# Performance work log

Hardware: AMD Instinct MI355X
Metric: run time of the kernel (lower is better)

The kernel has to match this reference:

```python
import jax, jax.numpy as jnp
import numpy as np

EMBED_DIM = 1024


def setup_inputs() -> dict:
    key = jax.random.key(0)
    ks = jax.random.split(key, 9)
    d = EMBED_DIM
    s = 1.0 / np.sqrt(d)
    x = jax.random.normal(ks[0], (4, 4096, d), dtype=jnp.float32)
    Wq = jax.random.normal(ks[1], (d, d), dtype=jnp.float32) * s
    bq = jax.random.normal(ks[2], (d,), dtype=jnp.float32) * 0.01
    Wk = jax.random.normal(ks[3], (d, d), dtype=jnp.float32) * s
    bk = jax.random.normal(ks[4], (d,), dtype=jnp.float32) * 0.01
    Wv = jax.random.normal(ks[5], (d, d), dtype=jnp.float32) * s
    bv = jax.random.normal(ks[6], (d,), dtype=jnp.float32) * 0.01
    Wo = jax.random.normal(ks[7], (d, d), dtype=jnp.float32) * s
    bo = jax.random.normal(ks[8], (d,), dtype=jnp.float32) * 0.01
    return {"x": x, "Wq": Wq, "bq": bq, "Wk": Wk, "bk": bk,
            "Wv": Wv, "bv": bv, "Wo": Wo, "bo": bo}


def reference(x, Wq, bq, Wk, bk, Wv, bv, Wo, bo):
    # x: [b, s, d]; single-head attention, scale = 1/sqrt(d)
    b, s, d = x.shape
    q = x @ Wq + bq
    k = x @ Wk + bk
    v = x @ Wv + bv
    scale = 1.0 / jnp.sqrt(jnp.asarray(d, x.dtype))
    scores = jnp.einsum('bqd,bkd->bqk', q, k) * scale  # [b, s, s]
    causal = jnp.tril(jnp.ones((s, s), dtype=bool))
    scores = jnp.where(causal, scores, jnp.asarray(-jnp.inf, scores.dtype))
    attn = jax.nn.softmax(scores, axis=-1)
    ctx = jnp.einsum('bqk,bkd->bqd', attn, v)
    return ctx @ Wo + bo
```

## Files before the change

kernel.cpp:

```cpp
#include <hip/hip_runtime.h>


typedef unsigned short u16;
typedef __attribute__((ext_vector_type(4))) unsigned short u16x4;
typedef __attribute__((ext_vector_type(8))) unsigned short u16x8;
typedef __attribute__((ext_vector_type(8))) __bf16 bf16x8;
typedef __attribute__((ext_vector_type(4))) float f32x4;

typedef const __attribute__((address_space(1))) void* as1cp;
typedef __attribute__((address_space(3))) void* as3p;

#define SBAR() __builtin_amdgcn_s_barrier()
#define SPIN() __builtin_amdgcn_sched_barrier(0)

struct GemmPtrs {
  const u16* A[4];
  const u16* B[4];
  const float* bias[4];
  void* C[4];
};
struct TransPtrs {
  const void* in[4];
  u16* out[4];
};
struct SmPtrs {
  u16* P[4];
};

__device__ __forceinline__ u16 f2bf(float f) {
  union { float f; unsigned int i; } c; c.f = f;
  unsigned int r = c.i + 0x7fffu + ((c.i >> 16) & 1u);
  return (u16)(r >> 16);
}
__device__ __forceinline__ float bf2f(u16 u) {
  union { unsigned int i; float f; } c; c.i = ((unsigned int)u) << 16;
  return c.f;
}

__global__ __launch_bounds__(256) void cast_f32_bf16(const float* __restrict__ in,
                                                     u16* __restrict__ out, int n4) {
  int i = blockIdx.x * blockDim.x + threadIdx.x;
  if (i >= n4) return;
  float4 v = ((const float4*)in)[i];
  u16x4 u;
  u.x = f2bf(v.x); u.y = f2bf(v.y); u.z = f2bf(v.z); u.w = f2bf(v.w);
  ((u16x4*)out)[i] = u;
}

template <bool IN_F32>
__global__ __launch_bounds__(256) void transpose_to_bf16(TransPtrs tp, int R, int C) {
  __shared__ u16 t[32][34];
  int z = blockIdx.z;
  int tx = threadIdx.x, ty = threadIdx.y;
  int c0 = blockIdx.x * 32, r0 = blockIdx.y * 32;
#pragma unroll
  for (int dy = 0; dy < 4; ++dy) {
    int r = r0 + ty + dy * 8;
    int c = c0 + tx;
    u16 hv;
    if (IN_F32) hv = f2bf(((const float*)tp.in[z])[(size_t)r * C + c]);
    else        hv = ((const u16*)tp.in[z])[(size_t)r * C + c];
    t[ty + dy * 8][tx] = hv;
  }
  __syncthreads();
  u16* op = tp.out[z];
#pragma unroll
  for (int dy = 0; dy < 4; ++dy) {
    int a = ty + dy * 8;
    op[(size_t)(c0 + a) * R + r0 + tx] = t[tx][a];
  }
}

__global__ __launch_bounds__(256) void softmax_causal(SmPtrs sp) {
  int row = blockIdx.x;
  u16* P = sp.P[blockIdx.y];
  int tid = threadIdx.x;
  int lane = tid & 63, wv = tid >> 6;
  u16x8* prow = (u16x8*)(P + (size_t)row * 4096);
  int nch = (row >> 3) + 1;
  int fend = ((row >> 7) + 1) << 4;
  int c0 = tid, c1 = tid + 256;
  bool a0 = c0 < nch, a1 = c1 < nch;
  float vals[16];
  float lmax = -3.0e38f;
  if (a0) {
    u16x8 u = prow[c0];
#pragma unroll
    for (int e = 0; e < 8; ++e) {
      float f = (c0 * 8 + e <= row) ? bf2f(u[e]) : -3.0e38f;
      vals[e] = f; lmax = fmaxf(lmax, f);
    }
  } else {
#pragma unroll
    for (int e = 0; e < 8; ++e) vals[e] = -3.0e38f;
  }
  if (a1) {
    u16x8 u = prow[c1];
#pragma unroll
    for (int e = 0; e < 8; ++e) {
      float f = (c1 * 8 + e <= row) ? bf2f(u[e]) : -3.0e38f;
      vals[8 + e] = f; lmax = fmaxf(lmax, f);
    }
  } else {
#pragma unroll
    for (int e = 0; e < 8; ++e) vals[8 + e] = -3.0e38f;
  }
  __shared__ float red[8];
#pragma unroll
  for (int off = 32; off > 0; off >>= 1) lmax = fmaxf(lmax, __shfl_down(lmax, off, 64));
  if (lane == 0) red[wv] = lmax;
  __syncthreads();
  float m2 = fmaxf(fmaxf(red[0], red[1]), fmaxf(red[2], red[3]));
  float lsum = 0.f;
#pragma unroll
  for (int e = 0; e < 16; ++e) {
    float ev = __expf(vals[e] - m2);
    vals[e] = ev;
    lsum += ev;
  }
#pragma unroll
  for (int off = 32; off > 0; off >>= 1) lsum += __shfl_down(lsum, off, 64);
  if (lane == 0) red[4 + wv] = lsum;
  __syncthreads();
  float inv = 1.0f / (red[4] + red[5] + red[6] + red[7]);
  if (a0) {
    u16x8 u;
#pragma unroll
    for (int e = 0; e < 8; ++e) u[e] = f2bf(vals[e] * inv);
    prow[c0] = u;
  }
  if (a1) {
    u16x8 u;
#pragma unroll
    for (int e = 0; e < 8; ++e) u[e] = f2bf(vals[8 + e] * inv);
    prow[c1] = u;
  }
  u16x8 zz = (u16x8)(u16)0;
  for (int c = nch + tid; c < fend; c += 256) prow[c] = zz;
}

template <int MODE, bool OUT_BF16, bool HAS_BIAS>
__global__ __launch_bounds__(512, 2) void gemm8ph(GemmPtrs p, int N, float cscale) {
  __shared__ __align__(16) u16 As[3][8192];
  __shared__ __align__(16) u16 Bs[3][8192];
  const int b = blockIdx.x;
  const int tid = threadIdx.x, lane = tid & 63, wv = tid >> 6;
  const int wm = (wv >> 2) << 7, wn = (wv & 3) << 6;
  const int lrow = lane & 15, lquad = lane >> 4;
  const int xs = (lquad ^ ((lrow >> 1) & 3)) << 3;
  const int aoff0 = (wm + lrow) * 32 + xs;
  const int boff0 = (wn + lrow) * 32 + xs;
  const int soff = (tid >> 2) * 1024 + (((tid & 3) ^ ((tid >> 3) & 3)) << 3);
  const int x = b & 7, u = b >> 3;
  const int nslot = (MODE == 1) ? (u < 4 ? 3 : 2) : (MODE == 0 ? 3 : 1);

  struct TP { const u16* A; const u16* B; int tm, tn, z; };
  auto tileOf = [&](int s) {
    TP t;
    if (MODE == 0) {
      int i = x * 32 + u;
      t.z = s; t.tm = (i >> 2) << 8; t.tn = (i & 3) << 8;
    } else if (MODE == 1) {
      int g = x * 68 + s * 32 + u;
      t.z = g / 136; int L = g - t.z * 136;
      int i = (int)((__fsqrt_rn(8.f * (float)L + 1.f) - 1.f) * 0.5f);
      while ((i + 1) * (i + 2) / 2 <= L) ++i;
      while (i * (i + 1) / 2 > L) --i;
      t.tm = i << 8; t.tn = (L - ((i * (i + 1)) >> 1)) << 8;
    } else {
      int i = x * 32 + u;
      t.z = 0; t.tm = (i >> 2) << 8; t.tn = (i & 3) << 8;
    }
    t.A = p.A[t.z] + (size_t)t.tm * 1024;
    t.B = p.B[t.z] + (size_t)t.tn * 1024;
    return t;
  };

  const u16* gA; const u16* gB; int stk = 0, sslot = 0;
  {
    TP t0 = tileOf(0);
    gA = t0.A + soff; gB = t0.B + soff;
  }
  auto adv = [&]() {
    gA += 32; gB += 32;
    if (++stk == 32) {
      stk = 0;
      if (++sslot < nslot) {
        TP t = tileOf(sslot);
        gA = t.A + soff; gB = t.B + soff;
      }
    }
  };
  auto stgA = [&](int s) __attribute__((always_inline)) {
    __builtin_amdgcn_global_load_lds((as1cp)gA, (as3p)(As[s] + wv * 512), 16, 0, 0);
    __builtin_amdgcn_global_load_lds((as1cp)(gA + 131072), (as3p)(As[s] + 4096 + wv * 512), 16, 0, 0);
  };
  auto stgB = [&](int s) __attribute__((always_inline)) {
    __builtin_amdgcn_global_load_lds((as1cp)gB, (as3p)(Bs[s] + wv * 512), 16, 0, 0);
    __builtin_amdgcn_global_load_lds((as1cp)(gB + 131072), (as3p)(Bs[s] + 4096 + wv * 512), 16, 0, 0);
    adv();
  };

  f32x4 acc[8][4];
#pragma unroll
  for (int i = 0; i < 8; ++i)
#pragma unroll
    for (int j = 0; j < 4; ++j) acc[i][j] = (f32x4){0.f, 0.f, 0.f, 0.f};

  auto epi = [&](int cs2) {
    TP t = tileOf(cs2);
    float bvv[4] = {0.f, 0.f, 0.f, 0.f};
    if constexpr (HAS_BIAS) {
#pragma unroll
      for (int n = 0; n < 4; ++n) bvv[n] = p.bias[t.z][t.tn + wn + n * 16 + lrow];
    }
#pragma unroll
    for (int m = 0; m < 8; ++m)
#pragma unroll
      for (int r = 0; r < 4; ++r) {
        size_t row = (size_t)(t.tm + wm + m * 16 + lquad * 4 + r);
#pragma unroll
        for (int n = 0; n < 4; ++n) {
          int col = t.tn + wn + n * 16 + lrow;
          float vvv = acc[m][n][r] * cscale + bvv[n];
          if (OUT_BF16) ((u16*)p.C[t.z])[row * N + col] = f2bf(vvv);
          else          ((float*)p.C[t.z])[row * N + col] = vvv;
        }
      }
#pragma unroll
    for (int m2 = 0; m2 < 8; ++m2)
#pragma unroll
      for (int n2 = 0; n2 < 4; ++n2) acc[m2][n2] = (f32x4){0.f, 0.f, 0.f, 0.f};
  };

  stgA(0); stgB(0);
  stgA(1); stgB(1);
  asm volatile("s_waitcnt vmcnt(4)");
  SBAR();
  SPIN();

  const int T = nslot * 32;
  int cs = 0, c = 0;
  for (int t = 0; t < T; ++t) {
    const int s = (c >= 1) ? c - 1 : 2;
    const bool stg = (t + 2) < T;
    bf16x8 af[4], bf[4];
#pragma unroll
    for (int m = 0; m < 4; ++m) af[m] = *(const bf16x8*)&As[c][aoff0 + m * 512];
#pragma unroll
    for (int n = 0; n < 4; ++n) bf[n] = *(const bf16x8*)&Bs[c][boff0 + n * 512];
    if (stg) stgA(s);
    SPIN();
    SBAR();
    asm volatile("s_waitcnt lgkmcnt(0)");
    SPIN();
    __builtin_amdgcn_s_setprio(1);
#pragma unroll
    for (int m = 0; m < 4; ++m)
#pragma unroll
      for (int n = 0; n < 4; ++n)
        acc[m][n] = __builtin_amdgcn_mfma_f32_16x16x32_bf16(af[m], bf[n], acc[m][n], 0, 0, 0);
    __builtin_amdgcn_s_setprio(0);
    SPIN();
    SBAR();
#pragma unroll
    for (int m = 0; m < 4; ++m) af[m] = *(const bf16x8*)&As[c][aoff0 + 2048 + m * 512];
    if (stg) stgB(s);
    SPIN();
    if (stg)               asm volatile("s_waitcnt vmcnt(4)");
    else if (t + 1 < T)    asm volatile("s_waitcnt vmcnt(0)");
    SBAR();
    asm volatile("s_waitcnt lgkmcnt(0)");
    SPIN();
    __builtin_amdgcn_s_setprio(1);
#pragma unroll
    for (int m = 0; m < 4; ++m)
#pragma unroll
      for (int n = 0; n < 4; ++n)
        acc[4 + m][n] = __builtin_amdgcn_mfma_f32_16x16x32_bf16(af[m], bf[n], acc[4 + m][n], 0, 0, 0);
    __builtin_amdgcn_s_setprio(0);
    SPIN();
    SBAR();
    if (((t + 1) & 31) == 0) { SPIN(); epi(cs); ++cs; }
    if (++c == 3) c = 0;
  }
}

__global__ __launch_bounds__(512, 2) void gemm_pv3(GemmPtrs p) {
  __shared__ __align__(16) u16 As[3][4096];
  __shared__ __align__(16) u16 Bs[3][8192];
  const int b = blockIdx.x;
  const int tid = threadIdx.x, lane = tid & 63, wv = tid >> 6;
  const int wm = (wv >> 2) << 6, wn = (wv & 3) << 6;
  const int lrow = lane & 15, lquad = lane >> 4;
  const int xs = (lquad ^ ((lrow >> 1) & 3)) << 3;
  const int aoff0 = (wm + lrow) * 32 + xs;
  const int boff0 = (wn + lrow) * 32 + xs;
  const int soff = (tid >> 2) * 4096 + (((tid & 3) ^ ((tid >> 3) & 3)) << 3);
  const int x = b & 7, u = b >> 3;
  const int P = x * 32 + u;
  const int z = P >> 6, j = (P >> 2) & 15, n4 = P & 3;
  const int i1 = j, i2 = 31 - j;
  const int tn = n4 << 8;
  const int T1 = (i1 + 1) * 4;
  const int niter1 = (i2 + 1) * 4;
  const u16* Abase = p.A[z];
  const u16* Bbase = p.B[z] + (size_t)tn * 4096;

  const u16* gA = Abase + (size_t)(i1 << 7) * 4096 + soff;
  const u16* gB = Bbase + soff;
  int stk = 0, sslot = 0;
  auto adv = [&]() {
    gA += 32; gB += 32;
    ++stk;
    if (sslot == 0 && stk == T1) {
      stk = 0; sslot = 1;
      gA = Abase + (size_t)(i2 << 7) * 4096 + soff;
      gB = Bbase + soff;
    } else if (sslot == 1 && stk == niter1) {
      stk = 0; sslot = 2;
    }
  };
  auto stage = [&](int s) __attribute__((always_inline)) {
    __builtin_amdgcn_global_load_lds((as1cp)gA, (as3p)(As[s] + wv * 512), 16, 0, 0);
    __builtin_amdgcn_global_load_lds((as1cp)gB, (as3p)(Bs[s] + wv * 512), 16, 0, 0);
    __builtin_amdgcn_global_load_lds((as1cp)(gB + 524288), (as3p)(Bs[s] + 4096 + wv * 512), 16, 0, 0);
    adv();
  };

  f32x4 acc[4][4];
#pragma unroll
  for (int i = 0; i < 4; ++i)
#pragma unroll
    for (int jj = 0; jj < 4; ++jj) acc[i][jj] = (f32x4){0.f, 0.f, 0.f, 0.f};

  auto epi = [&](int s) {
    int tm = (s ? i2 : i1) << 7;
#pragma unroll
    for (int m = 0; m < 4; ++m)
#pragma unroll
      for (int r = 0; r < 4; ++r) {
        size_t row = (size_t)(tm + wm + m * 16 + lquad * 4 + r);
#pragma unroll
        for (int n = 0; n < 4; ++n) {
          int col = tn + wn + n * 16 + lrow;
          ((u16*)p.C[z])[row * 1024 + col] = f2bf(acc[m][n][r]);
        }
      }
#pragma unroll
    for (int m2 = 0; m2 < 4; ++m2)
#pragma unroll
      for (int n2 = 0; n2 < 4; ++n2) acc[m2][n2] = (f32x4){0.f, 0.f, 0.f, 0.f};
  };

  stage(0); stage(1);
  asm volatile("s_waitcnt vmcnt(3)");
  SBAR();
  SPIN();

  const int T = 132;
  int c = 0;
  for (int t = 0; t < T; ++t) {
    const int s = (c >= 1) ? c - 1 : 2;
    const bool stg = (t + 2) < T;
    bf16x8 af[4], bf[4];
#pragma unroll
    for (int m = 0; m < 4; ++m) af[m] = *(const bf16x8*)&As[c][aoff0 + m * 512];
#pragma unroll
    for (int n = 0; n < 4; ++n) bf[n] = *(const bf16x8*)&Bs[c][boff0 + n * 512];
    if (stg) stage(s);
    SPIN();
    if (stg)            asm volatile("s_waitcnt vmcnt(3)");
    else if (t + 1 < T) asm volatile("s_waitcnt vmcnt(0)");
    SBAR();
    asm volatile("s_waitcnt lgkmcnt(0)");
    SPIN();
    __builtin_amdgcn_s_setprio(1);
#pragma unroll
    for (int m = 0; m < 4; ++m)
#pragma unroll
      for (int n = 0; n < 4; ++n)
        acc[m][n] = __builtin_amdgcn_mfma_f32_16x16x32_bf16(af[m], bf[n], acc[m][n], 0, 0, 0);
    __builtin_amdgcn_s_setprio(0);
    SPIN();
    SBAR();
    if (t + 1 == T1) { SPIN(); epi(0); }
    if (++c == 3) c = 0;
  }
  epi(1);
}

extern "C" void kernel_launch(void* const* d_in, const int* in_sizes, int n_in,
                              void* d_out, int out_size, void* d_ws, size_t ws_size,
                              hipStream_t stream) {
  const float* x  = (const float*)d_in[0];
  const float* Wq = (const float*)d_in[1];
  const float* bq = (const float*)d_in[2];
  const float* Wk = (const float*)d_in[3];
  const float* bk = (const float*)d_in[4];
  const float* Wv = (const float*)d_in[5];
  const float* bv = (const float*)d_in[6];
  const float* Wo = (const float*)d_in[7];
  const float* bo = (const float*)d_in[8];

  const int S = 4096, D = 1024;
  const size_t XE = (size_t)4 * S * D;
  const size_t BSE = (size_t)S * D;

  char* ws = (char*)d_ws;
  u16* xb  = (u16*)(ws + 0);
  u16* q   = (u16*)(ws + 33554432);
  u16* k   = (u16*)(ws + 67108864);
  u16* v   = (u16*)(ws + 100663296);
  u16* ctx = (u16*)(ws + 134217728);
  u16* wqT = (u16*)(ws + 167772160);
  u16* wkT = wqT + 1048576;
  u16* wvT = wkT + 1048576;
  u16* woT = wvT + 1048576;
  u16* attn2 = (u16*)(ws + 176160768);
  u16* attn0 = (u16*)d_out;
  u16* attn1 = attn0 + (size_t)S * S;
  u16* attn3 = v;
  u16* vT = xb;
  u16* attn[4] = {attn0, attn1, attn2, attn3};

  cast_f32_bf16<<<(int)(XE / 4 / 256), 256, 0, stream>>>(x, xb, (int)(XE / 4));
  {
    TransPtrs tp = {{Wq, Wk, Wv, Wo}, {wqT, wkT, wvT, woT}};
    transpose_to_bf16<true><<<dim3(32, 32, 4), dim3(32, 8), 0, stream>>>(tp, D, D);
  }
  {
    GemmPtrs gp = {{xb, xb, xb, xb}, {wqT, wkT, wvT, wqT},
                   {bq, bk, bv, bq}, {q, k, v, q}};
    gemm8ph<0, true, true><<<256, 512, 0, stream>>>(gp, D, 1.0f);
  }
  {
    TransPtrs tp = {{v, v + BSE, v + 2 * BSE, v + 3 * BSE},
                    {vT, vT + BSE, vT + 2 * BSE, vT + 3 * BSE}};
    transpose_to_bf16<false><<<dim3(D / 32, S / 32, 4), dim3(32, 8), 0, stream>>>(tp, S, D);
  }
  {
    GemmPtrs gp = {{q, q + BSE, q + 2 * BSE, q + 3 * BSE},
                   {k, k + BSE, k + 2 * BSE, k + 3 * BSE},
                   {nullptr, nullptr, nullptr, nullptr},
                   {attn[0], attn[1], attn[2], attn[3]}};
    gemm8ph<1, true, false><<<256, 512, 0, stream>>>(gp, S, 0.03125f);
  }
  {
    SmPtrs sp = {{attn[0], attn[1], attn[2], attn[3]}};
    softmax_causal<<<dim3(S, 4), 256, 0, stream>>>(sp);
  }
  {
    GemmPtrs gp = {{attn[0], attn[1], attn[2], attn[3]},
                   {vT, vT + BSE, vT + 2 * BSE, vT + 3 * BSE},
                   {nullptr, nullptr, nullptr, nullptr},
                   {ctx, ctx + BSE, ctx + 2 * BSE, ctx + 3 * BSE}};
    gemm_pv3<<<256, 512, 0, stream>>>(gp);
  }
  {
    GemmPtrs gp = {{ctx, ctx, ctx, ctx}, {woT, woT, woT, woT},
                   {bo, bo, bo, bo}, {d_out, d_out, d_out, d_out}};
    gemm8ph<3, false, true><<<256, 512, 0, stream>>>(gp, D, 1.0f);
  }
}
```

Baseline: 508.3 us.

## Fuse causal softmax into QK epilogue and PV prologue with per-tile statistics

Removes the standalone softmax pass over the score matrix. The QK GEMM epilogue now computes per-row, per-256-column-block max and sum-of-exp. A small combine kernel merges these into a row max and inverse sum. The PV GEMM then loads raw scores through registers, applies exp, normalisation and the causal mask, and writes the result to LDS before the MFMAs. This avoids a full read-modify-write of the bf16 score matrix. The cost is extra work in the epilogue (reductions, barriers) and exp work in the PV main loop, whose A operand is no longer staged with direct global-to-LDS async loads.

```diff
diff --git a/kernel.cpp b/kernel.cpp
--- a/kernel.cpp
+++ b/kernel.cpp
@@ -23,9 +23,6 @@
   const void* in[4];
   u16* out[4];
 };
-struct SmPtrs {
-  u16* P[4];
-};
 
 __device__ __forceinline__ u16 f2bf(float f) {
   union { float f; unsigned int i; } c; c.f = f;
@@ -71,78 +68,32 @@
   }
 }
 
-__global__ __launch_bounds__(256) void softmax_causal(SmPtrs sp) {
-  int row = blockIdx.x;
-  u16* P = sp.P[blockIdx.y];
-  int tid = threadIdx.x;
-  int lane = tid & 63, wv = tid >> 6;
-  u16x8* prow = (u16x8*)(P + (size_t)row * 4096);
-  int nch = (row >> 3) + 1;
-  int fend = ((row >> 7) + 1) << 4;
-  int c0 = tid, c1 = tid + 256;
-  bool a0 = c0 < nch, a1 = c1 < nch;
-  float vals[16];
-  float lmax = -3.0e38f;
-  if (a0) {
-    u16x8 u = prow[c0];
-#pragma unroll
-    for (int e = 0; e < 8; ++e) {
-      float f = (c0 * 8 + e <= row) ? bf2f(u[e]) : -3.0e38f;
-      vals[e] = f; lmax = fmaxf(lmax, f);
-    }
-  } else {
-#pragma unroll
-    for (int e = 0; e < 8; ++e) vals[e] = -3.0e38f;
-  }
-  if (a1) {
-    u16x8 u = prow[c1];
-#pragma unroll
-    for (int e = 0; e < 8; ++e) {
-      float f = (c1 * 8 + e <= row) ? bf2f(u[e]) : -3.0e38f;
-      vals[8 + e] = f; lmax = fmaxf(lmax, f);
-    }
-  } else {
-#pragma unroll
-    for (int e = 0; e < 8; ++e) vals[8 + e] = -3.0e38f;
-  }
-  __shared__ float red[8];
-#pragma unroll
-  for (int off = 32; off > 0; off >>= 1) lmax = fmaxf(lmax, __shfl_down(lmax, off, 64));
-  if (lane == 0) red[wv] = lmax;
-  __syncthreads();
-  float m2 = fmaxf(fmaxf(red[0], red[1]), fmaxf(red[2], red[3]));
-  float lsum = 0.f;
-#pragma unroll
-  for (int e = 0; e < 16; ++e) {
-    float ev = __expf(vals[e] - m2);
-    vals[e] = ev;
-    lsum += ev;
-  }
-#pragma unroll
-  for (int off = 32; off > 0; off >>= 1) lsum += __shfl_down(lsum, off, 64);
-  if (lane == 0) red[4 + wv] = lsum;
-  __syncthreads();
-  float inv = 1.0f / (red[4] + red[5] + red[6] + red[7]);
-  if (a0) {
-    u16x8 u;
-#pragma unroll
-    for (int e = 0; e < 8; ++e) u[e] = f2bf(vals[e] * inv);
-    prow[c0] = u;
-  }
-  if (a1) {
-    u16x8 u;
-#pragma unroll
-    for (int e = 0; e < 8; ++e) u[e] = f2bf(vals[8 + e] * inv);
-    prow[c1] = u;
-  }
-  u16x8 zz = (u16x8)(u16)0;
-  for (int c = nch + tid; c < fend; c += 256) prow[c] = zz;
+__global__ __launch_bounds__(256) void sm_combine(const float* __restrict__ gM,
+                                                  const float* __restrict__ gS,
+                                                  float* __restrict__ Mrow,
+                                                  float* __restrict__ Linv) {
+  int r = blockIdx.x * 256 + threadIdx.x;
+  int z = r >> 12, row = r & 4095;
+  int nb = (row >> 8) + 1;
+  float M = -3.0e38f;
+  for (int cb = 0; cb < nb; ++cb)
+    M = fmaxf(M, gM[(((z * 16 + cb) << 12)) + row]);
+  float L = 0.f;
+  for (int cb = 0; cb < nb; ++cb) {
+    float pm = gM[(((z * 16 + cb) << 12)) + row];
+    L += gS[(((z * 16 + cb) << 12)) + row] * __expf(pm - M);
+  }
+  Mrow[(z << 12) + row] = M;
+  Linv[(z << 12) + row] = 1.0f / L;
 }
 
 template <int MODE, bool OUT_BF16, bool HAS_BIAS>
-__global__ __launch_bounds__(512, 2) void gemm8ph(GemmPtrs p, int N, float cscale) {
+__global__ __launch_bounds__(512, 2) void gemm8ph(GemmPtrs p, int N, float cscale,
+                                                  float* gM, float* gS) {
   __shared__ __align__(16) u16 As[3][8192];
   __shared__ __align__(16) u16 Bs[3][8192];
+  __shared__ __align__(16) float smax[1024];
+  __shared__ __align__(16) float ssum[1024];
   const int b = blockIdx.x;
   const int tid = threadIdx.x, lane = tid & 63, wv = tid >> 6;
   const int wm = (wv >> 2) << 7, wn = (wv & 3) << 6;
@@ -209,6 +160,65 @@
 
   auto epi = [&](int cs2) {
     TP t = tileOf(cs2);
+    if constexpr (MODE == 1) {
+      const bool diag = (t.tm == t.tn);
+      const int wnidx = wv & 3;
+#pragma unroll
+      for (int m = 0; m < 8; ++m)
+#pragma unroll
+        for (int r = 0; r < 4; ++r) {
+          int rl = wm + m * 16 + lquad * 4 + r;
+          float mx = -3.0e38f;
+#pragma unroll
+          for (int n = 0; n < 4; ++n) {
+            float vb = bf2f(f2bf(acc[m][n][r] * cscale));
+            int cl = wn + n * 16 + lrow;
+            if (diag && cl > rl) vb = -3.0e38f;
+            mx = fmaxf(mx, vb);
+          }
+          mx = fmaxf(mx, __shfl_xor(mx, 1, 64));
+          mx = fmaxf(mx, __shfl_xor(mx, 2, 64));
+          mx = fmaxf(mx, __shfl_xor(mx, 4, 64));
+          mx = fmaxf(mx, __shfl_xor(mx, 8, 64));
+          if (lrow == 0) smax[rl * 4 + wnidx] = mx;
+        }
+      SBAR();
+#pragma unroll
+      for (int m = 0; m < 8; ++m)
+#pragma unroll
+        for (int r = 0; r < 4; ++r) {
+          int rl = wm + m * 16 + lquad * 4 + r;
+          f32x4 m4 = *(const f32x4*)&smax[rl * 4];
+          float Mt = fmaxf(fmaxf(m4[0], m4[1]), fmaxf(m4[2], m4[3]));
+          float sm = 0.f;
+#pragma unroll
+          for (int n = 0; n < 4; ++n) {
+            float vb = bf2f(f2bf(acc[m][n][r] * cscale));
+            int cl = wn + n * 16 + lrow;
+            if (diag && cl > rl) vb = -3.0e38f;
+            sm += __expf(vb - Mt);
+          }
+          sm += __shfl_xor(sm, 1, 64); sm += __shfl_xor(sm, 2, 64);
+          sm += __shfl_xor(sm, 4, 64); sm += __shfl_xor(sm, 8, 64);
+          if (lrow == 0) ssum[rl * 4 + wnidx] = sm;
+        }
+      SBAR();
+      if ((wv & 3) == 0) {
+#pragma unroll
+        for (int h = 0; h < 2; ++h) {
+          int rl = wm + h * 64 + lane;
+          f32x4 m4 = *(const f32x4*)&smax[rl * 4];
+          float Mt = fmaxf(fmaxf(m4[0], m4[1]), fmaxf(m4[2], m4[3]));
+          f32x4 s4 = *(const f32x4*)&ssum[rl * 4];
+          float L = (s4[0] + s4[1]) + (s4[2] + s4[3]);
+          int row_abs = t.tm + rl;
+          int cb = t.tn >> 8;
+          gM[((t.z * 16 + cb) << 12) + row_abs] = Mt;
+          gS[((t.z * 16 + cb) << 12) + row_abs] = L;
+        }
+      }
+      SBAR();
+    }
     float bvv[4] = {0.f, 0.f, 0.f, 0.f};
     if constexpr (HAS_BIAS) {
 #pragma unroll
@@ -286,7 +296,9 @@
   }
 }
 
-__global__ __launch_bounds__(512, 2) void gemm_pv3(GemmPtrs p) {
+__global__ __launch_bounds__(512, 2) void gemm_pvf(GemmPtrs p,
+                                                   const float* __restrict__ Mrow,
+                                                   const float* __restrict__ Linv) {
   __shared__ __align__(16) u16 As[3][4096];
   __shared__ __align__(16) u16 Bs[3][8192];
   const int b = blockIdx.x;
@@ -296,36 +308,57 @@
   const int xs = (lquad ^ ((lrow >> 1) & 3)) << 3;
   const int aoff0 = (wm + lrow) * 32 + xs;
   const int boff0 = (wn + lrow) * 32 + xs;
-  const int soff = (tid >> 2) * 4096 + (((tid & 3) ^ ((tid >> 3) & 3)) << 3);
+  const int jsw = (((tid & 3) ^ ((tid >> 3) & 3)) << 3);
+  const int soffB = (tid >> 2) * 4096 + jsw;
   const int x = b & 7, u = b >> 3;
   const int P = x * 32 + u;
   const int z = P >> 6, j = (P >> 2) & 15, n4 = P & 3;
   const int i1 = j, i2 = 31 - j;
   const int tn = n4 << 8;
   const int T1 = (i1 + 1) * 4;
-  const int niter1 = (i2 + 1) * 4;
+  const int T = 132;
+  const int T2 = T - T1;
   const u16* Abase = p.A[z];
   const u16* Bbase = p.B[z] + (size_t)tn * 4096;
 
-  const u16* gA = Abase + (size_t)(i1 << 7) * 4096 + soff;
-  const u16* gB = Bbase + soff;
-  int stk = 0, sslot = 0;
+  const int rloc = tid >> 2;
+  const int ra1 = (i1 << 7) + rloc, ra2 = (i2 << 7) + rloc;
+  const float M1 = Mrow[(z << 12) + ra1], L1i = Linv[(z << 12) + ra1];
+  const float M2 = Mrow[(z << 12) + ra2], L2i = Linv[(z << 12) + ra2];
+
+  const u16* gA = Abase + (size_t)ra1 * 4096 + jsw;
+  const u16* gB = Bbase + soffB;
+  int stk = 0;
   auto adv = [&]() {
     gA += 32; gB += 32;
-    ++stk;
-    if (sslot == 0 && stk == T1) {
-      stk = 0; sslot = 1;
-      gA = Abase + (size_t)(i2 << 7) * 4096 + soff;
-      gB = Bbase + soff;
-    } else if (sslot == 1 && stk == niter1) {
-      stk = 0; sslot = 2;
-    }
-  };
-  auto stage = [&](int s) __attribute__((always_inline)) {
-    __builtin_amdgcn_global_load_lds((as1cp)gA, (as3p)(As[s] + wv * 512), 16, 0, 0);
+    if (++stk == T1) {
+      gA = Abase + (size_t)ra2 * 4096 + jsw;
+      gB = Bbase + soffB;
+    }
+  };
+  auto stgB = [&](int s) __attribute__((always_inline)) {
     __builtin_amdgcn_global_load_lds((as1cp)gB, (as3p)(Bs[s] + wv * 512), 16, 0, 0);
     __builtin_amdgcn_global_load_lds((as1cp)(gB + 524288), (as3p)(Bs[s] + 4096 + wv * 512), 16, 0, 0);
-    adv();
+  };
+
+  auto xform = [&](int kt, int slot, u16x8 a8) __attribute__((always_inline)) {
+    const bool s2 = (kt >= T1);
+    const int klocal = s2 ? kt - T1 : kt;
+    const int Tseg = s2 ? T2 : T1;
+    const float M = s2 ? M2 : M1;
+    const float Li = s2 ? L2i : L1i;
+    const int rabs = s2 ? ra2 : ra1;
+    const int jb = klocal * 32 + jsw;
+    const bool dia = (klocal >= Tseg - 4);
+    u16x8 o;
+#pragma unroll
+    for (int e = 0; e < 8; ++e) {
+      float s = bf2f(a8[e]);
+      float pe = __expf(s - M) * Li;
+      if (dia && (jb + e > rabs)) pe = 0.f;
+      o[e] = f2bf(pe);
+    }
+    *(u16x8*)(As[slot] + tid * 8) = o;
   };
 
   f32x4 acc[4][4];
@@ -353,24 +386,37 @@
       for (int n2 = 0; n2 < 4; ++n2) acc[m2][n2] = (f32x4){0.f, 0.f, 0.f, 0.f};
   };
 
-  stage(0); stage(1);
-  asm volatile("s_waitcnt vmcnt(3)");
-  SBAR();
-  SPIN();
-
-  const int T = 132;
+  u16x8 aregP;
+  {
+    u16x8 a0 = *(const u16x8*)gA;
+    stgB(0); adv();
+    xform(0, 0, a0);
+    aregP = *(const u16x8*)gA;
+    stgB(1); adv();
+    SPIN();
+    asm volatile("s_waitcnt vmcnt(3)");
+    SBAR();
+    SPIN();
+  }
+
   int c = 0;
   for (int t = 0; t < T; ++t) {
-    const int s = (c >= 1) ? c - 1 : 2;
-    const bool stg = (t + 2) < T;
+    const int cnext = (c == 2) ? 0 : c + 1;
+    const int cstage = (c >= 1) ? c - 1 : 2;
     bf16x8 af[4], bf[4];
 #pragma unroll
     for (int m = 0; m < 4; ++m) af[m] = *(const bf16x8*)&As[c][aoff0 + m * 512];
 #pragma unroll
     for (int n = 0; n < 4; ++n) bf[n] = *(const bf16x8*)&Bs[c][boff0 + n * 512];
-    if (stg) stage(s);
-    SPIN();
-    if (stg)            asm volatile("s_waitcnt vmcnt(3)");
+    if (t + 1 < T) xform(t + 1, cnext, aregP);
+    if (t + 2 < T) {
+      aregP = *(const u16x8*)gA;
+      SPIN();
+      stgB(cstage);
+      adv();
+    }
+    SPIN();
+    if (t + 2 < T)      asm volatile("s_waitcnt vmcnt(3)");
     else if (t + 1 < T) asm volatile("s_waitcnt vmcnt(0)");
     SBAR();
     asm volatile("s_waitcnt lgkmcnt(0)");
@@ -385,7 +431,7 @@
     SPIN();
     SBAR();
     if (t + 1 == T1) { SPIN(); epi(0); }
-    if (++c == 3) c = 0;
+    c = cnext;
   }
   epi(1);
 }
@@ -423,6 +469,10 @@
   u16* attn3 = v;
   u16* vT = xb;
   u16* attn[4] = {attn0, attn1, attn2, attn3};
+  float* gM   = (float*)(ws + 134217728);
+  float* gS   = gM + (size_t)4 * 16 * 4096;
+  float* Mrow = (float*)(ws + 167772160);
+  float* LinvP = Mrow + (size_t)4 * 4096;
 
   cast_f32_bf16<<<(int)(XE / 4 / 256), 256, 0, stream>>>(x, xb, (int)(XE / 4));
   {
@@ -432,7 +482,7 @@
   {
     GemmPtrs gp = {{xb, xb, xb, xb}, {wqT, wkT, wvT, wqT},
                    {bq, bk, bv, bq}, {q, k, v, q}};
-    gemm8ph<0, true, true><<<256, 512, 0, stream>>>(gp, D, 1.0f);
+    gemm8ph<0, true, true><<<256, 512, 0, stream>>>(gp, D, 1.0f, nullptr, nullptr);
   }
   {
     TransPtrs tp = {{v, v + BSE, v + 2 * BSE, v + 3 * BSE},
@@ -444,22 +494,19 @@
                    {k, k + BSE, k + 2 * BSE, k + 3 * BSE},
                    {nullptr, nullptr, nullptr, nullptr},
                    {attn[0], attn[1], attn[2], attn[3]}};
-    gemm8ph<1, true, false><<<256, 512, 0, stream>>>(gp, S, 0.03125f);
-  }
-  {
-    SmPtrs sp = {{attn[0], attn[1], attn[2], attn[3]}};
-    softmax_causal<<<dim3(S, 4), 256, 0, stream>>>(sp);
-  }
+    gemm8ph<1, true, false><<<256, 512, 0, stream>>>(gp, S, 0.03125f, gM, gS);
+  }
+  sm_combine<<<64, 256, 0, stream>>>(gM, gS, Mrow, LinvP);
   {
     GemmPtrs gp = {{attn[0], attn[1], attn[2], attn[3]},
                    {vT, vT + BSE, vT + 2 * BSE, vT + 3 * BSE},
                    {nullptr, nullptr, nullptr, nullptr},
                    {ctx, ctx + BSE, ctx + 2 * BSE, ctx + 3 * BSE}};
-    gemm_pv3<<<256, 512, 0, stream>>>(gp);
+    gemm_pvf<<<256, 512, 0, stream>>>(gp, Mrow, LinvP);
   }
   {
     GemmPtrs gp = {{ctx, ctx, ctx, ctx}, {woT, woT, woT, woT},
                    {bo, bo, bo, bo}, {d_out, d_out, d_out, d_out}};
-    gemm8ph<3, false, true><<<256, 512, 0, stream>>>(gp, D, 1.0f);
-  }
-}
+    gemm8ph<3, false, true><<<256, 512, 0, stream>>>(gp, D, 1.0f, nullptr, nullptr);
+  }
+}
```

After: 725.2 us. +42.7%, slower.

## Split leftover causal QK tiles along K to balance block workload

Applied to the files above, without the earlier changes.

The QK^T GEMM previously gave a third full tile to 32 of 256 blocks, which made them the critical path. The 32 leftover tiles are now split in half along K across 64 blocks, which write fp32 partials to workspace. A new reduce kernel then sums the halves, applies the scale and stores bf16. This shortens the longest block's iteration count, at the cost of an extra launch and about 16 MB of fp32 partial traffic.

```diff
diff --git a/kernel.cpp b/kernel.cpp
--- a/kernel.cpp
+++ b/kernel.cpp
@@ -139,8 +139,31 @@
   for (int c = nch + tid; c < fend; c += 256) prow[c] = zz;
 }
 
+__global__ __launch_bounds__(256) void reduce_half(const float* __restrict__ part,
+                                                   SmPtrs sp, float scale) {
+  int idx = blockIdx.x * 256 + threadIdx.x;
+  int tile = idx >> 14;
+  int e4 = idx & 16383;
+  int r = e4 >> 6, c4 = (e4 & 63) << 2;
+  int x = tile >> 2, e = tile & 3;
+  int g = x * 68 + 64 + e;
+  int z = g / 136, L = g - z * 136;
+  int i = (int)((__fsqrt_rn(8.f * (float)L + 1.f) - 1.f) * 0.5f);
+  while ((i + 1) * (i + 2) / 2 <= L) ++i;
+  while (i * (i + 1) / 2 > L) --i;
+  int j = L - ((i * (i + 1)) >> 1);
+  const float* p0 = part + ((size_t)tile * 2) * 65536 + r * 256 + c4;
+  f32x4 a = *(const f32x4*)p0;
+  f32x4 b = *(const f32x4*)(p0 + 65536);
+  u16x4 o;
+#pragma unroll
+  for (int q = 0; q < 4; ++q) o[q] = f2bf((a[q] + b[q]) * scale);
+  *(u16x4*)(sp.P[z] + (size_t)(i * 256 + r) * 4096 + j * 256 + c4) = o;
+}
+
 template <int MODE, bool OUT_BF16, bool HAS_BIAS>
-__global__ __launch_bounds__(512, 2) void gemm8ph(GemmPtrs p, int N, float cscale) {
+__global__ __launch_bounds__(512, 2) void gemm8ph(GemmPtrs p, int N, float cscale,
+                                                  float* gPart) {
   __shared__ __align__(16) u16 As[3][8192];
   __shared__ __align__(16) u16 Bs[3][8192];
   const int b = blockIdx.x;
@@ -152,7 +175,8 @@
   const int boff0 = (wn + lrow) * 32 + xs;
   const int soff = (tid >> 2) * 1024 + (((tid & 3) ^ ((tid >> 3) & 3)) << 3);
   const int x = b & 7, u = b >> 3;
-  const int nslot = (MODE == 1) ? (u < 4 ? 3 : 2) : (MODE == 0 ? 3 : 1);
+  const int nslot = (MODE == 1) ? (u < 8 ? 3 : 2) : (MODE == 0 ? 3 : 1);
+  const int T = (MODE == 1) ? (u < 8 ? 80 : 64) : (MODE == 0 ? 96 : 32);
 
   struct TP { const u16* A; const u16* B; int tm, tn, z; };
   auto tileOf = [&](int s) {
@@ -160,19 +184,25 @@
     if (MODE == 0) {
       int i = x * 32 + u;
       t.z = s; t.tm = (i >> 2) << 8; t.tn = (i & 3) << 8;
+      t.A = p.A[t.z] + (size_t)t.tm * 1024;
+      t.B = p.B[t.z] + (size_t)t.tn * 1024;
     } else if (MODE == 1) {
-      int g = x * 68 + s * 32 + u;
+      int g, kh = 0;
+      if (s < 2) g = x * 68 + s * 32 + u;
+      else { g = x * 68 + 64 + (u >> 1); kh = u & 1; }
       t.z = g / 136; int L = g - t.z * 136;
       int i = (int)((__fsqrt_rn(8.f * (float)L + 1.f) - 1.f) * 0.5f);
       while ((i + 1) * (i + 2) / 2 <= L) ++i;
       while (i * (i + 1) / 2 > L) --i;
       t.tm = i << 8; t.tn = (L - ((i * (i + 1)) >> 1)) << 8;
+      t.A = p.A[t.z] + (size_t)t.tm * 1024 + kh * 512;
+      t.B = p.B[t.z] + (size_t)t.tn * 1024 + kh * 512;
     } else {
       int i = x * 32 + u;
       t.z = 0; t.tm = (i >> 2) << 8; t.tn = (i & 3) << 8;
-    }
-    t.A = p.A[t.z] + (size_t)t.tm * 1024;
-    t.B = p.B[t.z] + (size_t)t.tn * 1024;
+      t.A = p.A[t.z] + (size_t)t.tm * 1024;
+      t.B = p.B[t.z] + (size_t)t.tn * 1024;
+    }
     return t;
   };
 
@@ -183,7 +213,8 @@
   }
   auto adv = [&]() {
     gA += 32; gB += 32;
-    if (++stk == 32) {
+    const int nit = (MODE == 1 && sslot == 2) ? 16 : 32;
+    if (++stk == nit) {
       stk = 0;
       if (++sslot < nslot) {
         TP t = tileOf(sslot);
@@ -209,24 +240,37 @@
 
   auto epi = [&](int cs2) {
     TP t = tileOf(cs2);
-    float bvv[4] = {0.f, 0.f, 0.f, 0.f};
-    if constexpr (HAS_BIAS) {
-#pragma unroll
-      for (int n = 0; n < 4; ++n) bvv[n] = p.bias[t.z][t.tn + wn + n * 16 + lrow];
-    }
-#pragma unroll
-    for (int m = 0; m < 8; ++m)
-#pragma unroll
-      for (int r = 0; r < 4; ++r) {
-        size_t row = (size_t)(t.tm + wm + m * 16 + lquad * 4 + r);
-#pragma unroll
-        for (int n = 0; n < 4; ++n) {
-          int col = t.tn + wn + n * 16 + lrow;
-          float vvv = acc[m][n][r] * cscale + bvv[n];
-          if (OUT_BF16) ((u16*)p.C[t.z])[row * N + col] = f2bf(vvv);
-          else          ((float*)p.C[t.z])[row * N + col] = vvv;
+    if (MODE == 1 && cs2 == 2) {
+      float* dst = gPart + ((size_t)((x * 4 + (u >> 1)) * 2 + (u & 1))) * 65536;
+#pragma unroll
+      for (int m = 0; m < 8; ++m)
+#pragma unroll
+        for (int r = 0; r < 4; ++r) {
+          int row = wm + m * 16 + lquad * 4 + r;
+#pragma unroll
+          for (int n = 0; n < 4; ++n)
+            dst[row * 256 + wn + n * 16 + lrow] = acc[m][n][r];
         }
+    } else {
+      float bvv[4] = {0.f, 0.f, 0.f, 0.f};
+      if constexpr (HAS_BIAS) {
+#pragma unroll
+        for (int n = 0; n < 4; ++n) bvv[n] = p.bias[t.z][t.tn + wn + n * 16 + lrow];
       }
+#pragma unroll
+      for (int m = 0; m < 8; ++m)
+#pragma unroll
+        for (int r = 0; r < 4; ++r) {
+          size_t row = (size_t)(t.tm + wm + m * 16 + lquad * 4 + r);
+#pragma unroll
+          for (int n = 0; n < 4; ++n) {
+            int col = t.tn + wn + n * 16 + lrow;
+            float vvv = acc[m][n][r] * cscale + bvv[n];
+            if (OUT_BF16) ((u16*)p.C[t.z])[row * N + col] = f2bf(vvv);
+            else          ((float*)p.C[t.z])[row * N + col] = vvv;
+          }
+        }
+    }
 #pragma unroll
     for (int m2 = 0; m2 < 8; ++m2)
 #pragma unroll
@@ -239,8 +283,7 @@
   SBAR();
   SPIN();
 
-  const int T = nslot * 32;
-  int cs = 0, c = 0;
+  int cs = 0, c = 0, kend = 32;
   for (int t = 0; t < T; ++t) {
     const int s = (c >= 1) ? c - 1 : 2;
     const bool stg = (t + 2) < T;
@@ -281,7 +324,12 @@
     __builtin_amdgcn_s_setprio(0);
     SPIN();
     SBAR();
-    if (((t + 1) & 31) == 0) { SPIN(); epi(cs); ++cs; }
+    if (t + 1 == kend) {
+      SPIN();
+      epi(cs);
+      ++cs;
+      kend += (MODE == 1 && cs == 2) ? 16 : 32;
+    }
     if (++c == 3) c = 0;
   }
 }
@@ -423,6 +471,7 @@
   u16* attn3 = v;
   u16* vT = xb;
   u16* attn[4] = {attn0, attn1, attn2, attn3};
+  float* gPart = (float*)(ws + 134217728);
 
   cast_f32_bf16<<<(int)(XE / 4 / 256), 256, 0, stream>>>(x, xb, (int)(XE / 4));
   {
@@ -432,7 +481,7 @@
   {
     GemmPtrs gp = {{xb, xb, xb, xb}, {wqT, wkT, wvT, wqT},
                    {bq, bk, bv, bq}, {q, k, v, q}};
-    gemm8ph<0, true, true><<<256, 512, 0, stream>>>(gp, D, 1.0f);
+    gemm8ph<0, true, true><<<256, 512, 0, stream>>>(gp, D, 1.0f, nullptr);
   }
   {
     TransPtrs tp = {{v, v + BSE, v + 2 * BSE, v + 3 * BSE},
@@ -444,7 +493,11 @@
                    {k, k + BSE, k + 2 * BSE, k + 3 * BSE},
                    {nullptr, nullptr, nullptr, nullptr},
                    {attn[0], attn[1], attn[2], attn[3]}};
-    gemm8ph<1, true, false><<<256, 512, 0, stream>>>(gp, S, 0.03125f);
+    gemm8ph<1, true, false><<<256, 512, 0, stream>>>(gp, S, 0.03125f, gPart);
+  }
+  {
+    SmPtrs sp = {{attn[0], attn[1], attn[2], attn[3]}};
+    reduce_half<<<2048, 256, 0, stream>>>(gPart, sp, 0.03125f);
   }
   {
     SmPtrs sp = {{attn[0], attn[1], attn[2], attn[3]}};
@@ -460,6 +513,6 @@
   {
     GemmPtrs gp = {{ctx, ctx, ctx, ctx}, {woT, woT, woT, woT},
                    {bo, bo, bo, bo}, {d_out, d_out, d_out, d_out}};
-    gemm8ph<3, false, true><<<256, 512, 0, stream>>>(gp, D, 1.0f);
-  }
-}
+    gemm8ph<3, false, true><<<256, 512, 0, stream>>>(gp, D, 1.0f, nullptr);
+  }
+}
```

After: 553.1 us. +8.8%, slower.
